# Kernel optimization log

Hardware: AMD Instinct MI355X
Metric: run time of the kernel (lower is better)

## Reference

```python
import jax, jax.numpy as jnp
import numpy as np

D_MODEL = 1024
N_HEADS = 16
DK = D_MODEL // N_HEADS


def setup_inputs() -> dict:
    key = jax.random.key(0)
    k1, k2, k3, k4 = jax.random.split(key, 4)
    x = jax.random.normal(k1, (2, 2048, D_MODEL), dtype=jnp.float32)
    # torch nn.Linear stores weight as [out_features, in_features]
    W_qkv = jax.random.normal(k2, (3 * D_MODEL, D_MODEL), dtype=jnp.float32) * (1.0 / np.sqrt(D_MODEL))
    W_proj = jax.random.normal(k3, (D_MODEL, D_MODEL), dtype=jnp.float32) * (1.0 / np.sqrt(D_MODEL))
    b_proj = jax.random.normal(k4, (D_MODEL,), dtype=jnp.float32) * 0.01
    return {"x": x, "W_qkv": W_qkv, "W_proj": W_proj, "b_proj": b_proj}


def reference(x, W_qkv, W_proj, b_proj):
    B, L, D = x.shape
    qkv = x @ W_qkv.T                      # [B, L, 3D]
    q, k, v = jnp.split(qkv, 3, axis=-1)   # each [B, L, D]

    def split_heads(t):
        return t.reshape(B, L, N_HEADS, DK).transpose(0, 2, 1, 3)  # [B, H, L, dk]

    q, k, v = map(split_heads, (q, k, v))
    scale = jnp.float32(1.0 / np.sqrt(DK))
    scores = jnp.einsum('bhid,bhjd->bhij', q, k) * scale  # [B, H, L, L]
    attn = jax.nn.softmax(scores, axis=-1)
    out = jnp.einsum('bhij,bhjd->bhid', attn, v)           # [B, H, L, dk]
    out = out.transpose(0, 2, 1, 3).reshape(B, L, D)
    return out @ W_proj.T + b_proj
```

## Files before the change

kernel.cpp:

```cpp
#include <hip/hip_runtime.h>
#include <stdint.h>

typedef unsigned short ushort_t;
typedef __bf16 bf16x4 __attribute__((ext_vector_type(4)));
typedef __bf16 bf16x8 __attribute__((ext_vector_type(8)));
typedef float f32x4 __attribute__((ext_vector_type(4)));
typedef float f32x16 __attribute__((ext_vector_type(16)));
typedef unsigned short us8 __attribute__((ext_vector_type(8)));
typedef unsigned short us4v __attribute__((ext_vector_type(4)));

__device__ __forceinline__ float bf2f(ushort_t u) {
  union { uint32_t u; float f; } v; v.u = ((uint32_t)u) << 16; return v.f;
}
__device__ __forceinline__ ushort_t f2bf(float f) {
  union { float f; uint32_t u; } v; v.f = f;
  uint32_t u = v.u;
  uint32_t r = (u + 0x7FFFu + ((u >> 16) & 1u)) >> 16;
  return (ushort_t)r;
}
__device__ __forceinline__ uint32_t pkbf(float a, float b) {
  __bf16 x = (__bf16)a, y = (__bf16)b;
  uint32_t ux = __builtin_bit_cast(unsigned short, x);
  uint32_t uy = __builtin_bit_cast(unsigned short, y);
  return ux | (uy << 16);
}
__device__ __forceinline__ void gload_lds16(const void* g, void* l) {
  __builtin_amdgcn_global_load_lds(
      (const __attribute__((address_space(1))) void*)g,
      (__attribute__((address_space(3))) void*)l, 16, 0, 0);
}
__device__ __forceinline__ void tr2(const ushort_t* p, bf16x4& lo, bf16x4& hi) {
  asm volatile("ds_read_b64_tr_b16 %0, %2\n\t"
               "ds_read_b64_tr_b16 %1, %2 offset:128"
               : "=&v"(lo), "=&v"(hi)
               : "v"((const __attribute__((address_space(3))) ushort_t*)p));
}

template <typename T> __device__ __forceinline__ T to_out(float f);
template <> __device__ __forceinline__ ushort_t to_out<ushort_t>(float f) { return f2bf(f); }
template <> __device__ __forceinline__ float to_out<float>(float f) { return f; }

__global__ void f2b3_kernel(const float* __restrict__ a, ushort_t* __restrict__ ao, int na,
                            const float* __restrict__ b, ushort_t* __restrict__ bo, int nb,
                            const float* __restrict__ c, ushort_t* __restrict__ co, int nc) {
  int i = blockIdx.x * blockDim.x + threadIdx.x;
  int total = na + nb + nc;
  int stride = gridDim.x * blockDim.x;
  for (; i < total; i += stride) {
    const float* src; ushort_t* dst; int j = i;
    if (j < na) { src = a; dst = ao; }
    else if ((j -= na) < nb) { src = b; dst = bo; }
    else { j -= nb; src = c; dst = co; }
    float4 v = ((const float4*)src)[j];
    us4v o;
    o[0] = f2bf(v.x); o[1] = f2bf(v.y); o[2] = f2bf(v.z); o[3] = f2bf(v.w);
    ((us4v*)dst)[j] = o;
  }
}

template<bool BIAS, typename OT>
__global__ __launch_bounds__(256, 2) void gemm_bt(
    const ushort_t* __restrict__ A, const ushort_t* __restrict__ W,
    const float* __restrict__ bias, OT* __restrict__ C,
    int M, int N, int K)
{
  __shared__ ushort_t As[128 * 64];
  __shared__ ushort_t Bs[128 * 64];
  const int t = threadIdx.x;
  const int w = t >> 6, lane = t & 63;
  const int lg = lane >> 4, lc = lane & 15;
  const int rowbase = blockIdx.y * 128;
  const int colbase = blockIdx.x * 128;
  const int wr = (w >> 1) * 64, wc = (w & 1) * 64;

  f32x4 acc[4][4] = {};
  const int nkt = K >> 6;

  for (int kt = 0; kt < nkt; ++kt) {
#pragma unroll
    for (int i = 0; i < 4; ++i) {
      int off = (i * 256 + t) * 16;
      int row = off >> 7;
      int cb  = off & 127;
      int ec  = cb ^ ((row & 7) << 4);
      gload_lds16(A + (size_t)(rowbase + row) * K + kt * 64 + (ec >> 1),
                  (char*)As + off);
      gload_lds16(W + (size_t)(colbase + row) * K + kt * 64 + (ec >> 1),
                  (char*)Bs + off);
    }
    __syncthreads();
#pragma unroll
    for (int kk = 0; kk < 2; ++kk) {
      bf16x8 af[4], bf[4];
#pragma unroll
      for (int m = 0; m < 4; ++m) {
        int row = wr + m * 16 + lc;
        int kb  = (lg * 16 + kk * 64) ^ ((row & 7) << 4);
        af[m] = *(const bf16x8*)((const char*)As + row * 128 + kb);
        int col = wc + m * 16 + lc;
        int kb2 = (lg * 16 + kk * 64) ^ ((col & 7) << 4);
        bf[m] = *(const bf16x8*)((const char*)Bs + col * 128 + kb2);
      }
#pragma unroll
      for (int m = 0; m < 4; ++m)
#pragma unroll
        for (int n = 0; n < 4; ++n)
          acc[m][n] = __builtin_amdgcn_mfma_f32_16x16x32_bf16(af[m], bf[n],
                                                              acc[m][n], 0, 0, 0);
    }
    __syncthreads();
  }

#pragma unroll
  for (int m = 0; m < 4; ++m) {
    int r0 = rowbase + wr + m * 16 + lg * 4;
#pragma unroll
    for (int n = 0; n < 4; ++n) {
      int c0 = colbase + wc + n * 16 + lc;
      float bv = 0.f;
      if (BIAS) bv = bias[c0];
#pragma unroll
      for (int j = 0; j < 4; ++j)
        C[(size_t)(r0 + j) * N + c0] = to_out<OT>(acc[m][n][j] + bv);
    }
  }
}

__global__ __launch_bounds__(512, 4) void attn_fwd(
    const ushort_t* __restrict__ qkv, ushort_t* __restrict__ o1,
    ushort_t* __restrict__ o2, float* __restrict__ lbuf)
{
  __shared__ ushort_t Ks[2][64 * 64];
  __shared__ ushort_t Vs[2][64 * 64];

  const int t = threadIdx.x, w = t >> 6, lane = t & 63;
  const int l31 = lane & 31, hi = lane >> 5;
  const int lc = lane & 15;

  const int d = blockIdx.x;
  const int qt = (d >> 3) & 7;
  const int bhs = (d & 7) * 8 + (d >> 6);
  const int bh = bhs >> 1, split = bhs & 1;
  const int b = bh >> 4, h = bh & 15;

  const ushort_t* Qg = qkv + (size_t)(b * 2048) * 3072 + h * 64;
  const ushort_t* Kg = Qg + 1024 + (size_t)split * 1024 * 3072;
  const ushort_t* Vg = Qg + 2048 + (size_t)split * 1024 * 3072;

  auto stage_k = [&](ushort_t* Kd, int kt) {
    int off = t * 16;
    int row = off >> 7;
    int cb  = off & 127;
    int ec  = cb ^ ((row & 7) << 4);
    gload_lds16(Kg + (size_t)(kt * 64 + row) * 3072 + (ec >> 1),
                (char*)Kd + off);
  };
  const int vr  = t >> 3;
  const int vc0 = (t & 7) * 8;
  const int vdst = (vc0 >> 4) * 2048 + (vr >> 2) * 128 + (vr & 3) * 32 +
                   (vc0 & 8) * 2;

  const ushort_t* qrow_p = Qg + (size_t)(qt * 256 + w * 32 + l31) * 3072;
  bf16x8 qf[4];
#pragma unroll
  for (int kk = 0; kk < 4; ++kk)
    qf[kk] = *(const bf16x8*)(qrow_p + kk * 16 + hi * 8);

  stage_k(Ks[0], 0);
  {
    us8 v = *(const us8*)(Vg + (size_t)vr * 3072 + vc0);
    *(us8*)((char*)Vs[0] + vdst) = v;
  }
  __syncthreads();

  f32x16 oacc0 = {}, oacc1 = {};
  float l = 0.f;
  const float SC = 0.125f * 1.44269504088896f;
  const int m16 = (lane >> 4) & 1;

  int cur = 0;
  for (int kt = 0; kt < 16; ++kt) {
    us8 vnext;
    if (kt < 15) {
      stage_k(Ks[cur ^ 1], kt + 1);
      vnext = *(const us8*)(Vg + (size_t)((kt + 1) * 64 + vr) * 3072 + vc0);
    }

    const ushort_t* Kc = Ks[cur];
    f32x16 s0 = {}, s1 = {};
    __builtin_amdgcn_s_setprio(1);
#pragma unroll
    for (int kk = 0; kk < 4; ++kk) {
      int cbyte = (kk * 32 + hi * 16);
      int r0 = l31, r1 = 32 + l31;
      bf16x8 kf0 = *(const bf16x8*)((const char*)Kc + r0 * 128 +
                                    (cbyte ^ ((r0 & 7) << 4)));
      bf16x8 kf1 = *(const bf16x8*)((const char*)Kc + r1 * 128 +
                                    (cbyte ^ ((r1 & 7) << 4)));
      s0 = __builtin_amdgcn_mfma_f32_32x32x16_bf16(kf0, qf[kk], s0, 0, 0, 0);
      s1 = __builtin_amdgcn_mfma_f32_32x32x16_bf16(kf1, qf[kk], s1, 0, 0, 0);
    }
    __builtin_amdgcn_s_setprio(0);

#pragma unroll
    for (int i = 0; i < 16; ++i) {
      s0[i] = __builtin_amdgcn_exp2f(s0[i] * SC);
      s1[i] = __builtin_amdgcn_exp2f(s1[i] * SC);
    }
    float rs = (((s0[0] + s0[1]) + (s0[2] + s0[3])) +
                ((s0[4] + s0[5]) + (s0[6] + s0[7]))) +
               (((s0[8] + s0[9]) + (s0[10] + s0[11])) +
                ((s0[12] + s0[13]) + (s0[14] + s0[15])));
    float rt = (((s1[0] + s1[1]) + (s1[2] + s1[3])) +
                ((s1[4] + s1[5]) + (s1[6] + s1[7]))) +
               (((s1[8] + s1[9]) + (s1[10] + s1[11])) +
                ((s1[12] + s1[13]) + (s1[14] + s1[15])));
    rs += rt;
    rs += __shfl_xor(rs, 32);
    l += rs;

    uint32_t pk0[8], pk1[8];
#pragma unroll
    for (int j = 0; j < 8; ++j) {
      pk0[j] = pkbf(s0[2 * j], s0[2 * j + 1]);
      pk1[j] = pkbf(s1[2 * j], s1[2 * j + 1]);
    }

    if (kt < 15)
      *(us8*)((char*)Vs[cur ^ 1] + vdst) = vnext;

    const ushort_t* Vc = Vs[cur];
    bf16x8 pa[4], vf[4][2];
#pragma unroll
    for (int ks = 0; ks < 4; ++ks) {
      int j0 = 4 * (ks & 1);
      uint32_t x0 = (ks < 2) ? pk0[j0]     : pk1[j0];
      uint32_t x1 = (ks < 2) ? pk0[j0 + 1] : pk1[j0 + 1];
      uint32_t y0 = (ks < 2) ? pk0[j0 + 2] : pk1[j0 + 2];
      uint32_t y1 = (ks < 2) ? pk0[j0 + 3] : pk1[j0 + 3];
      asm volatile("v_permlane32_swap_b32 %0, %1" : "+v"(x0), "+v"(y0));
      asm volatile("v_permlane32_swap_b32 %0, %1" : "+v"(x1), "+v"(y1));
      union { uint32_t du[4]; bf16x8 v; } U;
      U.du[0] = x0; U.du[1] = x1; U.du[2] = y0; U.du[3] = y1;
      pa[ks] = U.v;
#pragma unroll
      for (int nd = 0; nd < 2; ++nd) {
        bf16x4 lo, hh;
        tr2(Vc + (nd * 2 + m16) * 1024 + (4 * ks + 2 * hi) * 64 + lc * 4, lo, hh);
        vf[ks][nd] = __builtin_shufflevector(lo, hh, 0, 1, 2, 3, 4, 5, 6, 7);
      }
    }
    asm volatile("s_waitcnt lgkmcnt(0)" ::: "memory");
    __builtin_amdgcn_sched_barrier(0);
    __builtin_amdgcn_s_setprio(1);
#pragma unroll
    for (int ks = 0; ks < 4; ++ks) {
      oacc0 = __builtin_amdgcn_mfma_f32_32x32x16_bf16(pa[ks], vf[ks][0], oacc0, 0, 0, 0);
      oacc1 = __builtin_amdgcn_mfma_f32_32x32x16_bf16(pa[ks], vf[ks][1], oacc1, 0, 0, 0);
    }
    __builtin_amdgcn_s_setprio(0);

    __syncthreads();
    cur ^= 1;
  }

  ushort_t* op = split ? o2 : o1;
#pragma unroll
  for (int r = 0; r < 16; ++r) {
    int crow = (r & 3) + 8 * (r >> 2) + 4 * hi;
    int qrow = qt * 256 + w * 32 + crow;
    size_t base = ((size_t)(b * 2048 + qrow)) * 1024 + h * 64 + l31;
    op[base]      = f2bf(oacc0[r]);
    op[base + 32] = f2bf(oacc1[r]);
  }
  if (hi == 0) {
    int qrow = qt * 256 + w * 32 + l31;
    lbuf[(size_t)split * 65536 + (size_t)(b * 2048 + qrow) * 16 + h] = l;
  }
}

__global__ void merge_kernel(ushort_t* __restrict__ o1,
                             const ushort_t* __restrict__ o2,
                             const float* __restrict__ lbuf) {
  int i = blockIdx.x * blockDim.x + threadIdx.x;
  int row = i >> 7;
  int col = (i & 127) * 8;
  int h = col >> 6;
  float l1 = lbuf[(size_t)row * 16 + h];
  float l2 = lbuf[65536 + (size_t)row * 16 + h];
  float inv = 1.f / (l1 + l2);
  us8 v1 = ((const us8*)o1)[i];
  us8 v2 = ((const us8*)o2)[i];
  us8 o;
#pragma unroll
  for (int j = 0; j < 8; ++j)
    o[j] = f2bf((bf2f(v1[j]) + bf2f(v2[j])) * inv);
  ((us8*)o1)[i] = o;
}

extern "C" void kernel_launch(void* const* d_in, const int* in_sizes, int n_in,
                              void* d_out, int out_size, void* d_ws, size_t ws_size,
                              hipStream_t stream) {
  const float* x     = (const float*)d_in[0];
  const float* Wqkv  = (const float*)d_in[1];
  const float* Wproj = (const float*)d_in[2];
  const float* bproj = (const float*)d_in[3];
  float* out = (float*)d_out;

  ushort_t* qkv   = (ushort_t*)d_ws;
  ushort_t* aout  = qkv   + (size_t)4096 * 3072;
  ushort_t* xb    = aout  + (size_t)4096 * 1024;
  ushort_t* wqb   = xb    + (size_t)4096 * 1024;
  ushort_t* wpb   = wqb   + (size_t)3072 * 1024;
  float*    lbuf  = (float*)(wpb + (size_t)1024 * 1024);

  dim3 blk(256);
  f2b3_kernel<<<2048, blk, 0, stream>>>(x, xb, 4096 * 1024 / 4,
                                        Wqkv, wqb, 3072 * 1024 / 4,
                                        Wproj, wpb, 1024 * 1024 / 4);

  gemm_bt<false, ushort_t><<<dim3(24, 32), blk, 0, stream>>>(
      xb, wqb, nullptr, qkv, 4096, 3072, 1024);
  attn_fwd<<<dim3(512), dim3(512), 0, stream>>>(qkv, aout, xb, lbuf);
  merge_kernel<<<2048, blk, 0, stream>>>(aout, xb, lbuf);
  gemm_bt<true, float><<<dim3(8, 32), blk, 0, stream>>>(
      aout, wpb, bproj, out, 4096, 1024, 1024);
}
```

Measured before the change: 114.0 us.

## Fuse split-KV merge into projection GEMM and fold softmax scale into QKV GEMM

```diff
diff --git a/kernel.cpp b/kernel.cpp
--- a/kernel.cpp
+++ b/kernel.cpp
@@ -40,29 +40,30 @@
 template <> __device__ __forceinline__ ushort_t to_out<ushort_t>(float f) { return f2bf(f); }
 template <> __device__ __forceinline__ float to_out<float>(float f) { return f; }
 
-__global__ void f2b3_kernel(const float* __restrict__ a, ushort_t* __restrict__ ao, int na,
-                            const float* __restrict__ b, ushort_t* __restrict__ bo, int nb,
-                            const float* __restrict__ c, ushort_t* __restrict__ co, int nc) {
-  int i = blockIdx.x * blockDim.x + threadIdx.x;
-  int total = na + nb + nc;
-  int stride = gridDim.x * blockDim.x;
-  for (; i < total; i += stride) {
-    const float* src; ushort_t* dst; int j = i;
-    if (j < na) { src = a; dst = ao; }
-    else if ((j -= na) < nb) { src = b; dst = bo; }
-    else { j -= nb; src = c; dst = co; }
-    float4 v = ((const float4*)src)[j];
+#define SCQ 0.1803368801111204f
+
+__global__ void f2b3_kernel(const float* __restrict__ a, ushort_t* __restrict__ ao,
+                            const float* __restrict__ b, ushort_t* __restrict__ bo,
+                            const float* __restrict__ c, ushort_t* __restrict__ co) {
+  int blk = blockIdx.x;
+  const float* src; ushort_t* dst; int n4, b0, nb;
+  if (blk < 1024)      { src = a; dst = ao; n4 = 1048576; b0 = blk;        nb = 1024; }
+  else if (blk < 1792) { src = b; dst = bo; n4 = 786432;  b0 = blk - 1024; nb = 768; }
+  else                 { src = c; dst = co; n4 = 262144;  b0 = blk - 1792; nb = 256; }
+  for (int i = b0 * 256 + threadIdx.x; i < n4; i += nb * 256) {
+    float4 v = ((const float4*)src)[i];
     us4v o;
     o[0] = f2bf(v.x); o[1] = f2bf(v.y); o[2] = f2bf(v.z); o[3] = f2bf(v.w);
-    ((us4v*)dst)[j] = o;
-  }
-}
-
-template<bool BIAS, typename OT>
+    ((us4v*)dst)[i] = o;
+  }
+}
+
+template<bool BIAS, typename OT, bool SCALEQ, bool MERGEA>
 __global__ __launch_bounds__(256, 2) void gemm_bt(
     const ushort_t* __restrict__ A, const ushort_t* __restrict__ W,
     const float* __restrict__ bias, OT* __restrict__ C,
-    int M, int N, int K)
+    int M, int N, int K,
+    const ushort_t* __restrict__ A2, const float* __restrict__ lb)
 {
   __shared__ ushort_t As[128 * 64];
   __shared__ ushort_t Bs[128 * 64];
@@ -83,8 +84,22 @@
       int row = off >> 7;
       int cb  = off & 127;
       int ec  = cb ^ ((row & 7) << 4);
-      gload_lds16(A + (size_t)(rowbase + row) * K + kt * 64 + (ec >> 1),
-                  (char*)As + off);
+      if constexpr (MERGEA) {
+        int drow = rowbase + row;
+        int kcol = kt * 64 + (cb >> 1);
+        us8 v1 = *(const us8*)(A  + (size_t)drow * K + kcol);
+        us8 v2 = *(const us8*)(A2 + (size_t)drow * K + kcol);
+        float inv = 1.f / (lb[(size_t)drow * 16 + (kcol >> 6)] +
+                           lb[65536 + (size_t)drow * 16 + (kcol >> 6)]);
+        us8 o;
+#pragma unroll
+        for (int j = 0; j < 8; ++j)
+          o[j] = f2bf((bf2f(v1[j]) + bf2f(v2[j])) * inv);
+        *(us8*)((char*)As + (off ^ ((row & 7) << 4))) = o;
+      } else {
+        gload_lds16(A + (size_t)(rowbase + row) * K + kt * 64 + (ec >> 1),
+                    (char*)As + off);
+      }
       gload_lds16(W + (size_t)(colbase + row) * K + kt * 64 + (ec >> 1),
                   (char*)Bs + off);
     }
@@ -119,9 +134,11 @@
       int c0 = colbase + wc + n * 16 + lc;
       float bv = 0.f;
       if (BIAS) bv = bias[c0];
+      float qs = 1.f;
+      if (SCALEQ) qs = (c0 < 1024) ? SCQ : 1.f;
 #pragma unroll
       for (int j = 0; j < 4; ++j)
-        C[(size_t)(r0 + j) * N + c0] = to_out<OT>(acc[m][n][j] + bv);
+        C[(size_t)(r0 + j) * N + c0] = to_out<OT>(acc[m][n][j] * qs + bv);
     }
   }
 }
@@ -175,7 +192,6 @@
 
   f32x16 oacc0 = {}, oacc1 = {};
   float l = 0.f;
-  const float SC = 0.125f * 1.44269504088896f;
   const int m16 = (lane >> 4) & 1;
 
   int cur = 0;
@@ -204,8 +220,8 @@
 
 #pragma unroll
     for (int i = 0; i < 16; ++i) {
-      s0[i] = __builtin_amdgcn_exp2f(s0[i] * SC);
-      s1[i] = __builtin_amdgcn_exp2f(s1[i] * SC);
+      s0[i] = __builtin_amdgcn_exp2f(s0[i]);
+      s1[i] = __builtin_amdgcn_exp2f(s1[i]);
     }
     float rs = (((s0[0] + s0[1]) + (s0[2] + s0[3])) +
                 ((s0[4] + s0[5]) + (s0[6] + s0[7]))) +
@@ -215,9 +231,7 @@
                 ((s1[4] + s1[5]) + (s1[6] + s1[7]))) +
                (((s1[8] + s1[9]) + (s1[10] + s1[11])) +
                 ((s1[12] + s1[13]) + (s1[14] + s1[15])));
-    rs += rt;
-    rs += __shfl_xor(rs, 32);
-    l += rs;
+    l += rs + rt;
 
     uint32_t pk0[8], pk1[8];
 #pragma unroll
@@ -264,6 +278,8 @@
     cur ^= 1;
   }
 
+  l += __shfl_xor(l, 32);
+
   ushort_t* op = split ? o2 : o1;
 #pragma unroll
   for (int r = 0; r < 16; ++r) {
@@ -277,25 +293,6 @@
     int qrow = qt * 256 + w * 32 + l31;
     lbuf[(size_t)split * 65536 + (size_t)(b * 2048 + qrow) * 16 + h] = l;
   }
-}
-
-__global__ void merge_kernel(ushort_t* __restrict__ o1,
-                             const ushort_t* __restrict__ o2,
-                             const float* __restrict__ lbuf) {
-  int i = blockIdx.x * blockDim.x + threadIdx.x;
-  int row = i >> 7;
-  int col = (i & 127) * 8;
-  int h = col >> 6;
-  float l1 = lbuf[(size_t)row * 16 + h];
-  float l2 = lbuf[65536 + (size_t)row * 16 + h];
-  float inv = 1.f / (l1 + l2);
-  us8 v1 = ((const us8*)o1)[i];
-  us8 v2 = ((const us8*)o2)[i];
-  us8 o;
-#pragma unroll
-  for (int j = 0; j < 8; ++j)
-    o[j] = f2bf((bf2f(v1[j]) + bf2f(v2[j])) * inv);
-  ((us8*)o1)[i] = o;
 }
 
 extern "C" void kernel_launch(void* const* d_in, const int* in_sizes, int n_in,
@@ -308,21 +305,18 @@
   float* out = (float*)d_out;
 
   ushort_t* qkv   = (ushort_t*)d_ws;
-  ushort_t* aout  = qkv   + (size_t)4096 * 3072;
-  ushort_t* xb    = aout  + (size_t)4096 * 1024;
+  ushort_t* o1    = qkv   + (size_t)4096 * 3072;
+  ushort_t* xb    = o1    + (size_t)4096 * 1024;
   ushort_t* wqb   = xb    + (size_t)4096 * 1024;
   ushort_t* wpb   = wqb   + (size_t)3072 * 1024;
   float*    lbuf  = (float*)(wpb + (size_t)1024 * 1024);
 
   dim3 blk(256);
-  f2b3_kernel<<<2048, blk, 0, stream>>>(x, xb, 4096 * 1024 / 4,
-                                        Wqkv, wqb, 3072 * 1024 / 4,
-                                        Wproj, wpb, 1024 * 1024 / 4);
-
-  gemm_bt<false, ushort_t><<<dim3(24, 32), blk, 0, stream>>>(
-      xb, wqb, nullptr, qkv, 4096, 3072, 1024);
-  attn_fwd<<<dim3(512), dim3(512), 0, stream>>>(qkv, aout, xb, lbuf);
-  merge_kernel<<<2048, blk, 0, stream>>>(aout, xb, lbuf);
-  gemm_bt<true, float><<<dim3(8, 32), blk, 0, stream>>>(
-      aout, wpb, bproj, out, 4096, 1024, 1024);
-}
+  f2b3_kernel<<<2048, blk, 0, stream>>>(x, xb, Wqkv, wqb, Wproj, wpb);
+
+  gemm_bt<false, ushort_t, true, false><<<dim3(24, 32), blk, 0, stream>>>(
+      xb, wqb, nullptr, qkv, 4096, 3072, 1024, nullptr, nullptr);
+  attn_fwd<<<dim3(512), dim3(512), 0, stream>>>(qkv, o1, xb, lbuf);
+  gemm_bt<true, float, false, true><<<dim3(8, 32), blk, 0, stream>>>(
+      o1, wpb, bproj, out, 4096, 1024, 1024, xb, lbuf);
+}
```

After: 134.7 us. +18.2%, slower.
